# Kernel optimization log

Hardware: AMD Instinct MI355X
Metric: run time of the kernel (lower is better)

The kernel has to match this reference:

```python
import jax, jax.numpy as jnp
import numpy as np

DEC_HIDDEN = 512


def setup_inputs() -> dict:
    key = jax.random.key(0)
    k1, k2, k3, k4 = jax.random.split(key, 4)
    B, S, DEC, ENC2 = 32, 2048, 512, 1024
    s = jax.random.normal(k1, (1, B, DEC), dtype=jnp.float32)
    enc_output = jax.random.normal(k2, (B, S, ENC2), dtype=jnp.float32)
    # nn.Linear weights: attn [dec_hidden, enc_hidden*2 + dec_hidden], v [1, dec_hidden]
    W_attn = jax.random.normal(k3, (DEC, DEC + ENC2), dtype=jnp.float32) * (1.0 / np.sqrt(DEC + ENC2))
    W_v = jax.random.normal(k4, (1, DEC), dtype=jnp.float32) * (1.0 / np.sqrt(DEC))
    return {"s": s, "enc_output": enc_output, "W_attn": W_attn, "W_v": W_v}


def reference(s, enc_output, W_attn, W_v):
    # s: [1, B, D] -> [B, D]; enc_output: [B, S, 2E]
    s = jnp.squeeze(s, axis=0)
    dec = s.shape[-1]
    # torch.cat((s_repeated, enc_output), dim=2) @ W_attn.T, computed without
    # materializing the repeat/concat: split W_attn by column blocks.
    W_s = W_attn[:, :dec]       # [D, D]   (columns matching s)
    W_e = W_attn[:, dec:]       # [D, 2E]  (columns matching enc_output)
    # energy: [B, S, D]
    energy = jnp.tanh(
        jnp.einsum('bd,hd->bh', s, W_s)[:, None, :]
        + jnp.einsum('bse,he->bsh', enc_output, W_e)
    )
    # atten: [B, S]
    atten = jnp.einsum('bsh,h->bs', energy, W_v[0])
    soft_attn_weights = jax.nn.softmax(atten, axis=1)
    # context: [B, 2E]
    context = jnp.einsum('bs,bse->be', soft_attn_weights, enc_output)
    return (context, soft_attn_weights)
```

## Files before the change

### kernel.cpp

```cpp
#include <hip/hip_runtime.h>
#include <hip/hip_bf16.h>


typedef __attribute__((ext_vector_type(8))) short bf16x8;
typedef __attribute__((ext_vector_type(4))) float f32x4;

#define SB0() __builtin_amdgcn_sched_barrier(0)

static __device__ __forceinline__ unsigned short f2bf(float f) {
    union { float f; unsigned u; } v; v.f = f;
    unsigned r = (v.u + 0x7fffu + ((v.u >> 16) & 1u)) >> 16;
    return (unsigned short)r;
}

static __device__ __forceinline__ unsigned pk2(float x, float y) {
    union { __hip_bfloat162 h; unsigned u; } c;
    c.h = __float22bfloat162_rn(make_float2(x, y));
    return c.u;
}

static __device__ __forceinline__ float fast_tanh(float x) {
    return 1.0f - 2.0f / (__expf(2.0f * x) + 1.0f);
}

__global__ __launch_bounds__(256) void prep_sw(const float* __restrict__ s,
                                               const float* __restrict__ Wat,
                                               float* __restrict__ sW) {
    int id = blockIdx.x * 256 + threadIdx.x;
    int b = id >> 9, h = id & 511;
    const float4* wr = (const float4*)(Wat + (size_t)h * 1536);
    const float4* sr = (const float4*)(s + (size_t)b * 512);
    float acc = 0.f;
#pragma unroll 8
    for (int i = 0; i < 128; ++i) {
        float4 w = wr[i], sv = sr[i];
        acc += w.x * sv.x + w.y * sv.y + w.z * sv.z + w.w * sv.w;
    }
    sW[id] = acc;
}

__global__ __launch_bounds__(256) void prep_weB(const float* __restrict__ Wat,
                                                unsigned short* __restrict__ WebfB) {
    int tid = blockIdx.x * 256 + threadIdx.x;
    int lane = tid & 63;
    int g = tid >> 6;
    int nf = g & 3, wc = (g >> 2) & 3, kk = (g >> 4) & 1, step = (g >> 5) & 15, ct = (g >> 9) & 1;
    int col = ct * 256 + wc * 64 + nf * 16 + (lane & 15);
    int k0 = step * 64 + kk * 32 + (lane >> 4) * 8;
    const float* src = Wat + (size_t)col * 1536 + 512 + k0;
    float4 w0 = *(const float4*)src;
    float4 w1 = *(const float4*)(src + 4);
    union { unsigned short us[8]; int4 v; } p;
    p.us[0] = f2bf(w0.x); p.us[1] = f2bf(w0.y); p.us[2] = f2bf(w0.z); p.us[3] = f2bf(w0.w);
    p.us[4] = f2bf(w1.x); p.us[5] = f2bf(w1.y); p.us[6] = f2bf(w1.z); p.us[7] = f2bf(w1.w);
    *(int4*)(WebfB + (size_t)tid * 8) = p.v;
}

__global__ __launch_bounds__(256, 3) void energy_kernel(
    const float* __restrict__ enc, const unsigned short* __restrict__ WebfB,
    const float* __restrict__ sW, const float* __restrict__ Wv,
    float* __restrict__ attpart) {
    __shared__ __align__(16) unsigned short lT0[4096];
    __shared__ __align__(16) unsigned short lT1[4096];
    __shared__ float lred[4][64];

    const int t = threadIdx.x;
    const int lane = t & 63;
    const int wc = t >> 6;
    const int bid = blockIdx.x;
    const int ct = (bid >> 3) & 1;
    const int rt = (bid & 7) | ((bid >> 4) << 3);
    const int m0 = rt * 64;
    const int b = m0 >> 11;
    const int l15 = lane & 15;
    const int lkg = lane >> 4;

    const int arow = t >> 4;
    const int achk = t & 15;
    const float* aptr = enc + (size_t)(m0 + arow) * 1024 + achk * 4;
    const int wsw = (((achk >> 1) ^ (arow & 7)) << 4) | ((achk & 1) << 3);

    const int rrowbase = l15 * 128;
    const int rsw0 = (lkg ^ (l15 & 7)) << 4;
    const int rsw1 = ((4 + lkg) ^ (l15 & 7)) << 4;

    const unsigned short* wBbase = WebfB + (size_t)ct * 262144 + lane * 8;

    f32x4 acc[4][4];
#pragma unroll
    for (int mf = 0; mf < 4; ++mf)
#pragma unroll
        for (int nf = 0; nf < 4; ++nf) acc[mf][nf] = (f32x4){0.f, 0.f, 0.f, 0.f};

    float4 aregA[4], aregB[4];
    bf16x8 bfr[8];

#define LOADA(STEP, AR)                                                        \
    do {                                                                       \
        _Pragma("unroll")                                                      \
        for (int q = 0; q < 4; ++q)                                            \
            AR[q] = *(const float4*)(aptr + (size_t)q * 16384 + (STEP) * 64);  \
    } while (0)

#define LOADB(I)                                                               \
    do {                                                                       \
        _Pragma("unroll")                                                      \
        for (int kk = 0; kk < 2; ++kk)                                         \
            _Pragma("unroll")                                                  \
            for (int nf = 0; nf < 4; ++nf)                                     \
                bfr[kk * 4 + nf] = *(const bf16x8*)(                           \
                    wBbase + (size_t)((((I) * 2 + kk) * 4 + wc) * 4 + nf) * 512); \
    } while (0)

#define CVTW(AR, BUF)                                                          \
    do {                                                                       \
        _Pragma("unroll")                                                      \
        for (int q = 0; q < 4; ++q) {                                          \
            uint2 wv;                                                          \
            wv.x = pk2(AR[q].x, AR[q].y);                                      \
            wv.y = pk2(AR[q].z, AR[q].w);                                      \
            *(uint2*)((char*)(BUF) + (q * 16 + arow) * 128 + wsw) = wv;        \
        }                                                                      \
    } while (0)

#define COMP(BUF)                                                              \
    do {                                                                       \
        _Pragma("unroll")                                                      \
        for (int kk = 0; kk < 2; ++kk) {                                       \
            const int rs = kk ? rsw1 : rsw0;                                   \
            _Pragma("unroll")                                                  \
            for (int mf = 0; mf < 4; ++mf) {                                   \
                bf16x8 af = *(const bf16x8*)((const char*)(BUF) + rrowbase +   \
                                             mf * 2048 + rs);                  \
                _Pragma("unroll")                                              \
                for (int nf = 0; nf < 4; ++nf)                                 \
                    acc[mf][nf] = __builtin_amdgcn_mfma_f32_16x16x32_bf16(     \
                        af, bfr[kk * 4 + nf], acc[mf][nf], 0, 0, 0);           \
            }                                                                  \
        }                                                                      \
    } while (0)

#define BARRIER()                                              \
    do {                                                       \
        asm volatile("s_waitcnt lgkmcnt(0)" ::: "memory");     \
        __builtin_amdgcn_s_barrier();                          \
    } while (0)

#define STEP_FULL(I, CUR, NXT, AUSE, ALOAD)    \
    do {                                       \
        LOADB(I); SB0();                       \
        LOADA((I) + 2, ALOAD); SB0();          \
        CVTW(AUSE, NXT); SB0();                \
        __builtin_amdgcn_s_setprio(1);         \
        COMP(CUR);                             \
        __builtin_amdgcn_s_setprio(0);         \
        BARRIER();                             \
    } while (0)

    LOADA(0, aregA); SB0();
    LOADA(1, aregB); SB0();
    CVTW(aregA, lT0);
    BARRIER();

#pragma unroll 1
    for (int i = 0; i < 14; i += 2) {
        STEP_FULL(i, lT0, lT1, aregB, aregA);
        STEP_FULL(i + 1, lT1, lT0, aregA, aregB);
    }
    LOADB(14); SB0();
    CVTW(aregB, lT1); SB0();
    __builtin_amdgcn_s_setprio(1);
    COMP(lT0);
    __builtin_amdgcn_s_setprio(0);
    BARRIER();
    LOADB(15); SB0();
    __builtin_amdgcn_s_setprio(1);
    COMP(lT1);
    __builtin_amdgcn_s_setprio(0);

    float sWv[4], wvv[4];
#pragma unroll
    for (int nf = 0; nf < 4; ++nf) {
        int col = ct * 256 + wc * 64 + nf * 16 + l15;
        sWv[nf] = sW[(b << 9) + col];
        wvv[nf] = Wv[col];
    }
    float pa[4][4];
#pragma unroll
    for (int mf = 0; mf < 4; ++mf) {
#pragma unroll
        for (int r = 0; r < 4; ++r) pa[mf][r] = 0.f;
#pragma unroll
        for (int nf = 0; nf < 4; ++nf)
#pragma unroll
            for (int r = 0; r < 4; ++r)
                pa[mf][r] += fast_tanh(acc[mf][nf][r] + sWv[nf]) * wvv[nf];
    }
#pragma unroll
    for (int m = 1; m < 16; m <<= 1)
#pragma unroll
        for (int mf = 0; mf < 4; ++mf)
#pragma unroll
            for (int r = 0; r < 4; ++r)
                pa[mf][r] += __shfl_xor(pa[mf][r], m, 64);

    if (l15 == 0) {
#pragma unroll
        for (int mf = 0; mf < 4; ++mf)
#pragma unroll
            for (int r = 0; r < 4; ++r)
                lred[wc][mf * 16 + lkg * 4 + r] = pa[mf][r];
    }
    __syncthreads();
    if (t < 64) {
        attpart[(size_t)ct * 65536 + m0 + t] =
            (lred[0][t] + lred[1][t]) + (lred[2][t] + lred[3][t]);
    }
#undef LOADA
#undef LOADB
#undef CVTW
#undef COMP
#undef BARRIER
#undef STEP_FULL
}

__global__ __launch_bounds__(256) void softmax_kernel(const float* __restrict__ attpart,
                                                      float* __restrict__ out) {
    int b = blockIdx.x, t = threadIdx.x;
    float v[8];
#pragma unroll
    for (int i = 0; i < 8; ++i) {
        int idx = b * 2048 + t + 256 * i;
        v[i] = attpart[idx] + attpart[65536 + idx];
    }
    float mx = v[0];
#pragma unroll
    for (int i = 1; i < 8; ++i) mx = fmaxf(mx, v[i]);
#pragma unroll
    for (int m = 1; m < 64; m <<= 1) mx = fmaxf(mx, __shfl_xor(mx, m, 64));
    __shared__ float redm[4], reds[4];
    if ((t & 63) == 0) redm[t >> 6] = mx;
    __syncthreads();
    mx = fmaxf(fmaxf(redm[0], redm[1]), fmaxf(redm[2], redm[3]));
    float sum = 0.f;
#pragma unroll
    for (int i = 0; i < 8; ++i) { v[i] = __expf(v[i] - mx); sum += v[i]; }
#pragma unroll
    for (int m = 1; m < 64; m <<= 1) sum += __shfl_xor(sum, m, 64);
    if ((t & 63) == 0) reds[t >> 6] = sum;
    __syncthreads();
    sum = reds[0] + reds[1] + reds[2] + reds[3];
    float inv = 1.0f / sum;
    float* soft = out + 32768;
#pragma unroll
    for (int i = 0; i < 8; ++i) soft[b * 2048 + t + 256 * i] = v[i] * inv;
}

__global__ __launch_bounds__(256) void ctx_partial(const float* __restrict__ enc,
                                                   const float* __restrict__ soft,
                                                   float* __restrict__ part) {
    int blk = blockIdx.x;
    int b = blk >> 4, s0 = (blk & 15) * 128;
    int t = threadIdx.x;
    float4 a = {0.f, 0.f, 0.f, 0.f};
    const float* base = enc + ((size_t)(b * 2048 + s0)) * 1024 + t * 4;
    const float* sw = soft + b * 2048 + s0;
#pragma unroll 4
    for (int s = 0; s < 128; ++s) {
        float w = sw[s];
        float4 e = *(const float4*)(base + (size_t)s * 1024);
        a.x += w * e.x; a.y += w * e.y; a.z += w * e.z; a.w += w * e.w;
    }
    *(float4*)(part + (size_t)blk * 1024 + t * 4) = a;
}

__global__ __launch_bounds__(256) void ctx_reduce(const float* __restrict__ part,
                                                  float* __restrict__ ctx) {
    int id = blockIdx.x * 256 + threadIdx.x;
    int b = id >> 10, e = id & 1023;
    float s = 0.f;
#pragma unroll 8
    for (int c = 0; c < 16; ++c) s += part[((size_t)(b * 16 + c)) * 1024 + e];
    ctx[id] = s;
}

extern "C" void kernel_launch(void* const* d_in, const int* in_sizes, int n_in,
                              void* d_out, int out_size, void* d_ws, size_t ws_size,
                              hipStream_t stream) {
    const float* s   = (const float*)d_in[0];
    const float* enc = (const float*)d_in[1];
    const float* Wat = (const float*)d_in[2];
    const float* Wv  = (const float*)d_in[3];
    float* out = (float*)d_out;

    char* ws = (char*)d_ws;
    float* sW             = (float*)ws;
    unsigned short* WebfB = (unsigned short*)(ws + (64 << 10));
    float* attpart        = (float*)(ws + (64 << 10) + (1 << 20));
    float* part           = (float*)(ws + (64 << 10) + (1 << 20) + (512 << 10));

    prep_sw<<<64, 256, 0, stream>>>(s, Wat, sW);
    prep_weB<<<2048, 256, 0, stream>>>(Wat, WebfB);
    energy_kernel<<<2048, 256, 0, stream>>>(enc, WebfB, sW, Wv, attpart);
    softmax_kernel<<<32, 256, 0, stream>>>(attpart, out);
    ctx_partial<<<512, 256, 0, stream>>>(enc, out + 32768, part);
    ctx_reduce<<<128, 256, 0, stream>>>(part, out);
}
```

Before: 168.1 us.

## Stage energy-kernel weight tiles into LDS via async global_load_lds double buffering

```diff
diff --git a/kernel.cpp b/kernel.cpp
--- a/kernel.cpp
+++ b/kernel.cpp
@@ -4,8 +4,12 @@
 
 typedef __attribute__((ext_vector_type(8))) short bf16x8;
 typedef __attribute__((ext_vector_type(4))) float f32x4;
+typedef __attribute__((address_space(3))) unsigned lds_u32;
+typedef const __attribute__((address_space(1))) unsigned g_u32;
 
 #define SB0() __builtin_amdgcn_sched_barrier(0)
+#define PRIO1 __builtin_amdgcn_s_setprio(1)
+#define PRIO0 __builtin_amdgcn_s_setprio(0)
 
 static __device__ __forceinline__ unsigned short f2bf(float f) {
     union { float f; unsigned u; } v; v.f = f;
@@ -56,13 +60,16 @@
     *(int4*)(WebfB + (size_t)tid * 8) = p.v;
 }
 
-__global__ __launch_bounds__(256, 3) void energy_kernel(
+__global__ __launch_bounds__(256, 2) void energy_kernel(
     const float* __restrict__ enc, const unsigned short* __restrict__ WebfB,
     const float* __restrict__ sW, const float* __restrict__ Wv,
     float* __restrict__ attpart) {
-    __shared__ __align__(16) unsigned short lT0[4096];
-    __shared__ __align__(16) unsigned short lT1[4096];
-    __shared__ float lred[4][64];
+    __shared__ __align__(16) char smem[81920];
+    unsigned short* lT0 = (unsigned short*)smem;
+    unsigned short* lT1 = (unsigned short*)(smem + 8192);
+    char* Bb0 = smem + 16384;
+    char* Bb1 = smem + 49152;
+    float* lred = (float*)smem;
 
     const int t = threadIdx.x;
     const int lane = t & 63;
@@ -84,7 +91,7 @@
     const int rsw0 = (lkg ^ (l15 & 7)) << 4;
     const int rsw1 = ((4 + lkg) ^ (l15 & 7)) << 4;
 
-    const unsigned short* wBbase = WebfB + (size_t)ct * 262144 + lane * 8;
+    const char* gB = (const char*)WebfB + (size_t)ct * 524288;
 
     f32x4 acc[4][4];
 #pragma unroll
@@ -92,91 +99,88 @@
 #pragma unroll
         for (int nf = 0; nf < 4; ++nf) acc[mf][nf] = (f32x4){0.f, 0.f, 0.f, 0.f};
 
-    float4 aregA[4], aregB[4];
-    bf16x8 bfr[8];
-
-#define LOADA(STEP, AR)                                                        \
+    float4 azA[4], azB[4];
+
+#define BSTAGE(I, BB)                                                          \
+    do {                                                                       \
+        _Pragma("unroll")                                                      \
+        for (int q = 0; q < 8; ++q)                                            \
+            __builtin_amdgcn_global_load_lds(                                  \
+                (g_u32*)(gB + (size_t)(I) * 32768 + q * 4096 + wc * 1024 +     \
+                         lane * 16),                                           \
+                (lds_u32*)((BB) + q * 4096 + wc * 1024), 16, 0, 0);            \
+    } while (0)
+
+#define LOADA(S, AR)                                                           \
     do {                                                                       \
         _Pragma("unroll")                                                      \
         for (int q = 0; q < 4; ++q)                                            \
-            AR[q] = *(const float4*)(aptr + (size_t)q * 16384 + (STEP) * 64);  \
-    } while (0)
-
-#define LOADB(I)                                                               \
-    do {                                                                       \
-        _Pragma("unroll")                                                      \
-        for (int kk = 0; kk < 2; ++kk)                                         \
-            _Pragma("unroll")                                                  \
-            for (int nf = 0; nf < 4; ++nf)                                     \
-                bfr[kk * 4 + nf] = *(const bf16x8*)(                           \
-                    wBbase + (size_t)((((I) * 2 + kk) * 4 + wc) * 4 + nf) * 512); \
-    } while (0)
-
-#define CVTW(AR, BUF)                                                          \
+            AR[q] = *(const float4*)(aptr + (size_t)q * 16384 + (S) * 64);     \
+    } while (0)
+
+#define CVTW(AR, LT)                                                           \
     do {                                                                       \
         _Pragma("unroll")                                                      \
         for (int q = 0; q < 4; ++q) {                                          \
             uint2 wv;                                                          \
             wv.x = pk2(AR[q].x, AR[q].y);                                      \
             wv.y = pk2(AR[q].z, AR[q].w);                                      \
-            *(uint2*)((char*)(BUF) + (q * 16 + arow) * 128 + wsw) = wv;        \
+            *(uint2*)((char*)(LT) + (q * 16 + arow) * 128 + wsw) = wv;         \
         }                                                                      \
     } while (0)
 
-#define COMP(BUF)                                                              \
+#define COMP(LT, BB)                                                           \
     do {                                                                       \
         _Pragma("unroll")                                                      \
         for (int kk = 0; kk < 2; ++kk) {                                       \
             const int rs = kk ? rsw1 : rsw0;                                   \
             _Pragma("unroll")                                                  \
             for (int mf = 0; mf < 4; ++mf) {                                   \
-                bf16x8 af = *(const bf16x8*)((const char*)(BUF) + rrowbase +   \
+                bf16x8 af = *(const bf16x8*)((const char*)(LT) + rrowbase +    \
                                              mf * 2048 + rs);                  \
                 _Pragma("unroll")                                              \
-                for (int nf = 0; nf < 4; ++nf)                                 \
+                for (int nf = 0; nf < 4; ++nf) {                               \
+                    bf16x8 bf = *(const bf16x8*)(                              \
+                        (BB) + (kk * 16 + wc * 4 + nf) * 1024 + lane * 16);    \
                     acc[mf][nf] = __builtin_amdgcn_mfma_f32_16x16x32_bf16(     \
-                        af, bfr[kk * 4 + nf], acc[mf][nf], 0, 0, 0);           \
+                        af, bf, acc[mf][nf], 0, 0, 0);                         \
+                }                                                              \
             }                                                                  \
         }                                                                      \
     } while (0)
 
-#define BARRIER()                                              \
-    do {                                                       \
-        asm volatile("s_waitcnt lgkmcnt(0)" ::: "memory");     \
-        __builtin_amdgcn_s_barrier();                          \
-    } while (0)
-
-#define STEP_FULL(I, CUR, NXT, AUSE, ALOAD)    \
-    do {                                       \
-        LOADB(I); SB0();                       \
-        LOADA((I) + 2, ALOAD); SB0();          \
-        CVTW(AUSE, NXT); SB0();                \
-        __builtin_amdgcn_s_setprio(1);         \
-        COMP(CUR);                             \
-        __builtin_amdgcn_s_setprio(0);         \
-        BARRIER();                             \
-    } while (0)
-
-    LOADA(0, aregA); SB0();
-    LOADA(1, aregB); SB0();
-    CVTW(aregA, lT0);
-    BARRIER();
+#define ENDSTEP(N)                                                             \
+    do {                                                                       \
+        asm volatile("s_waitcnt vmcnt(" #N ") lgkmcnt(0)" ::: "memory");       \
+        SB0();                                                                 \
+        __builtin_amdgcn_s_barrier();                                          \
+    } while (0)
+
+    BSTAGE(0, Bb0); SB0();
+    LOADA(0, azA); SB0();
+    LOADA(1, azB); SB0();
+    CVTW(azA, lT0);
+    ENDSTEP(4);
 
 #pragma unroll 1
-    for (int i = 0; i < 14; i += 2) {
-        STEP_FULL(i, lT0, lT1, aregB, aregA);
-        STEP_FULL(i + 1, lT1, lT0, aregA, aregB);
-    }
-    LOADB(14); SB0();
-    CVTW(aregB, lT1); SB0();
-    __builtin_amdgcn_s_setprio(1);
-    COMP(lT0);
-    __builtin_amdgcn_s_setprio(0);
-    BARRIER();
-    LOADB(15); SB0();
-    __builtin_amdgcn_s_setprio(1);
-    COMP(lT1);
-    __builtin_amdgcn_s_setprio(0);
+    for (int k = 0; k < 7; ++k) {
+        const int i = 2 * k;
+        BSTAGE(i + 1, Bb1); SB0();
+        LOADA(i + 2, azA); SB0();
+        CVTW(azB, lT1); SB0();
+        PRIO1; COMP(lT0, Bb0); PRIO0;
+        ENDSTEP(4);
+        BSTAGE(i + 2, Bb0); SB0();
+        LOADA(i + 3, azB); SB0();
+        CVTW(azA, lT0); SB0();
+        PRIO1; COMP(lT1, Bb1); PRIO0;
+        ENDSTEP(4);
+    }
+    BSTAGE(15, Bb1); SB0();
+    CVTW(azB, lT1); SB0();
+    PRIO1; COMP(lT0, Bb0); PRIO0;
+    ENDSTEP(0);
+    PRIO1; COMP(lT1, Bb1); PRIO0;
 
     float sWv[4], wvv[4];
 #pragma unroll
@@ -204,24 +208,25 @@
             for (int r = 0; r < 4; ++r)
                 pa[mf][r] += __shfl_xor(pa[mf][r], m, 64);
 
+    __syncthreads();
     if (l15 == 0) {
 #pragma unroll
         for (int mf = 0; mf < 4; ++mf)
 #pragma unroll
             for (int r = 0; r < 4; ++r)
-                lred[wc][mf * 16 + lkg * 4 + r] = pa[mf][r];
+                lred[wc * 64 + mf * 16 + lkg * 4 + r] = pa[mf][r];
     }
     __syncthreads();
     if (t < 64) {
         attpart[(size_t)ct * 65536 + m0 + t] =
-            (lred[0][t] + lred[1][t]) + (lred[2][t] + lred[3][t]);
-    }
+            (lred[0 * 64 + t] + lred[1 * 64 + t]) +
+            (lred[2 * 64 + t] + lred[3 * 64 + t]);
+    }
+#undef BSTAGE
 #undef LOADA
-#undef LOADB
 #undef CVTW
 #undef COMP
-#undef BARRIER
-#undef STEP_FULL
+#undef ENDSTEP
 }
 
 __global__ __launch_bounds__(256) void softmax_kernel(const float* __restrict__ attpart,
@@ -300,7 +305,7 @@
     float* part           = (float*)(ws + (64 << 10) + (1 << 20) + (512 << 10));
 
     prep_sw<<<64, 256, 0, stream>>>(s, Wat, sW);
-    prep_weB<<<2048, 256, 0, stream>>>(Wat, WebfB);
+    prep_weB<<<256, 256, 0, stream>>>(Wat, WebfB);
     energy_kernel<<<2048, 256, 0, stream>>>(enc, WebfB, sW, Wv, attpart);
     softmax_kernel<<<32, 256, 0, stream>>>(attpart, out);
     ctx_partial<<<512, 256, 0, stream>>>(enc, out + 32768, part);
```

Result: slower. 190.5 us (+13.3%).

## Shrink energy tile to 64x128 with two-wave blocks and trim prep_weB grid

Applied to the files above, without the earlier changes.

```diff
diff --git a/kernel.cpp b/kernel.cpp
--- a/kernel.cpp
+++ b/kernel.cpp
@@ -6,6 +6,8 @@
 typedef __attribute__((ext_vector_type(4))) float f32x4;
 
 #define SB0() __builtin_amdgcn_sched_barrier(0)
+#define PRIO1 __builtin_amdgcn_s_setprio(1)
+#define PRIO0 __builtin_amdgcn_s_setprio(0)
 
 static __device__ __forceinline__ unsigned short f2bf(float f) {
     union { float f; unsigned u; } v; v.f = f;
@@ -56,35 +58,37 @@
     *(int4*)(WebfB + (size_t)tid * 8) = p.v;
 }
 
-__global__ __launch_bounds__(256, 3) void energy_kernel(
+__global__ __launch_bounds__(128, 4) void energy_kernel(
     const float* __restrict__ enc, const unsigned short* __restrict__ WebfB,
     const float* __restrict__ sW, const float* __restrict__ Wv,
     float* __restrict__ attpart) {
     __shared__ __align__(16) unsigned short lT0[4096];
     __shared__ __align__(16) unsigned short lT1[4096];
-    __shared__ float lred[4][64];
+    __shared__ float lred[2][64];
 
     const int t = threadIdx.x;
     const int lane = t & 63;
     const int wc = t >> 6;
     const int bid = blockIdx.x;
-    const int ct = (bid >> 3) & 1;
-    const int rt = (bid & 7) | ((bid >> 4) << 3);
+    const int ct = (bid >> 3) & 3;
+    const int rt = (bid & 7) | ((bid >> 5) << 3);
     const int m0 = rt * 64;
     const int b = m0 >> 11;
     const int l15 = lane & 15;
     const int lkg = lane >> 4;
+    const int ct2 = ct >> 1;
+    const int wc4 = (ct & 1) * 2 + wc;
 
     const int arow = t >> 4;
     const int achk = t & 15;
     const float* aptr = enc + (size_t)(m0 + arow) * 1024 + achk * 4;
-    const int wsw = (((achk >> 1) ^ (arow & 7)) << 4) | ((achk & 1) << 3);
+    const int wsw = (((achk >> 1) ^ arow) << 4) | ((achk & 1) << 3);
 
     const int rrowbase = l15 * 128;
     const int rsw0 = (lkg ^ (l15 & 7)) << 4;
     const int rsw1 = ((4 + lkg) ^ (l15 & 7)) << 4;
 
-    const unsigned short* wBbase = WebfB + (size_t)ct * 262144 + lane * 8;
+    const unsigned short* wB = WebfB + (size_t)ct2 * 262144 + lane * 8;
 
     f32x4 acc[4][4];
 #pragma unroll
@@ -92,14 +96,14 @@
 #pragma unroll
         for (int nf = 0; nf < 4; ++nf) acc[mf][nf] = (f32x4){0.f, 0.f, 0.f, 0.f};
 
-    float4 aregA[4], aregB[4];
+    float4 areg[8];
     bf16x8 bfr[8];
 
-#define LOADA(STEP, AR)                                                        \
-    do {                                                                       \
-        _Pragma("unroll")                                                      \
-        for (int q = 0; q < 4; ++q)                                            \
-            AR[q] = *(const float4*)(aptr + (size_t)q * 16384 + (STEP) * 64);  \
+#define LOADA(S)                                                               \
+    do {                                                                       \
+        _Pragma("unroll")                                                      \
+        for (int q = 0; q < 8; ++q)                                            \
+            areg[q] = *(const float4*)(aptr + (size_t)q * 8192 + (S) * 64);    \
     } while (0)
 
 #define LOADB(I)                                                               \
@@ -109,28 +113,28 @@
             _Pragma("unroll")                                                  \
             for (int nf = 0; nf < 4; ++nf)                                     \
                 bfr[kk * 4 + nf] = *(const bf16x8*)(                           \
-                    wBbase + (size_t)((((I) * 2 + kk) * 4 + wc) * 4 + nf) * 512); \
-    } while (0)
-
-#define CVTW(AR, BUF)                                                          \
-    do {                                                                       \
-        _Pragma("unroll")                                                      \
-        for (int q = 0; q < 4; ++q) {                                          \
+                    wB + (size_t)((((I) * 2 + kk) * 4 + wc4) * 4 + nf) * 512); \
+    } while (0)
+
+#define CVTW(LT)                                                               \
+    do {                                                                       \
+        _Pragma("unroll")                                                      \
+        for (int q = 0; q < 8; ++q) {                                          \
             uint2 wv;                                                          \
-            wv.x = pk2(AR[q].x, AR[q].y);                                      \
-            wv.y = pk2(AR[q].z, AR[q].w);                                      \
-            *(uint2*)((char*)(BUF) + (q * 16 + arow) * 128 + wsw) = wv;        \
+            wv.x = pk2(areg[q].x, areg[q].y);                                  \
+            wv.y = pk2(areg[q].z, areg[q].w);                                  \
+            *(uint2*)((char*)(LT) + (q * 8 + arow) * 128 + wsw) = wv;          \
         }                                                                      \
     } while (0)
 
-#define COMP(BUF)                                                              \
+#define COMP(LT)                                                               \
     do {                                                                       \
         _Pragma("unroll")                                                      \
         for (int kk = 0; kk < 2; ++kk) {                                       \
             const int rs = kk ? rsw1 : rsw0;                                   \
             _Pragma("unroll")                                                  \
             for (int mf = 0; mf < 4; ++mf) {                                   \
-                bf16x8 af = *(const bf16x8*)((const char*)(BUF) + rrowbase +   \
+                bf16x8 af = *(const bf16x8*)((const char*)(LT) + rrowbase +    \
                                              mf * 2048 + rs);                  \
                 _Pragma("unroll")                                              \
                 for (int nf = 0; nf < 4; ++nf)                                 \
@@ -146,42 +150,29 @@
         __builtin_amdgcn_s_barrier();                          \
     } while (0)
 
-#define STEP_FULL(I, CUR, NXT, AUSE, ALOAD)    \
-    do {                                       \
-        LOADB(I); SB0();                       \
-        LOADA((I) + 2, ALOAD); SB0();          \
-        CVTW(AUSE, NXT); SB0();                \
-        __builtin_amdgcn_s_setprio(1);         \
-        COMP(CUR);                             \
-        __builtin_amdgcn_s_setprio(0);         \
-        BARRIER();                             \
-    } while (0)
-
-    LOADA(0, aregA); SB0();
-    LOADA(1, aregB); SB0();
-    CVTW(aregA, lT0);
+    LOADA(0); SB0();
+    CVTW(lT0);
+    LOADA(1); SB0();
     BARRIER();
 
+    unsigned short* cur = lT0;
+    unsigned short* nxt = lT1;
 #pragma unroll 1
-    for (int i = 0; i < 14; i += 2) {
-        STEP_FULL(i, lT0, lT1, aregB, aregA);
-        STEP_FULL(i + 1, lT1, lT0, aregA, aregB);
-    }
-    LOADB(14); SB0();
-    CVTW(aregB, lT1); SB0();
-    __builtin_amdgcn_s_setprio(1);
-    COMP(lT0);
-    __builtin_amdgcn_s_setprio(0);
-    BARRIER();
+    for (int i = 0; i < 15; ++i) {
+        LOADB(i); SB0();
+        CVTW(nxt); SB0();
+        if (i < 14) { LOADA(i + 2); SB0(); }
+        PRIO1; COMP(cur); PRIO0;
+        BARRIER();
+        { unsigned short* tp = cur; cur = nxt; nxt = tp; }
+    }
     LOADB(15); SB0();
-    __builtin_amdgcn_s_setprio(1);
-    COMP(lT1);
-    __builtin_amdgcn_s_setprio(0);
+    PRIO1; COMP(cur); PRIO0;
 
     float sWv[4], wvv[4];
 #pragma unroll
     for (int nf = 0; nf < 4; ++nf) {
-        int col = ct * 256 + wc * 64 + nf * 16 + l15;
+        int col = ct * 128 + wc * 64 + nf * 16 + l15;
         sWv[nf] = sW[(b << 9) + col];
         wvv[nf] = Wv[col];
     }
@@ -213,15 +204,13 @@
     }
     __syncthreads();
     if (t < 64) {
-        attpart[(size_t)ct * 65536 + m0 + t] =
-            (lred[0][t] + lred[1][t]) + (lred[2][t] + lred[3][t]);
+        attpart[(size_t)ct * 65536 + m0 + t] = lred[0][t] + lred[1][t];
     }
 #undef LOADA
 #undef LOADB
 #undef CVTW
 #undef COMP
 #undef BARRIER
-#undef STEP_FULL
 }
 
 __global__ __launch_bounds__(256) void softmax_kernel(const float* __restrict__ attpart,
@@ -231,7 +220,8 @@
 #pragma unroll
     for (int i = 0; i < 8; ++i) {
         int idx = b * 2048 + t + 256 * i;
-        v[i] = attpart[idx] + attpart[65536 + idx];
+        v[i] = (attpart[idx] + attpart[65536 + idx]) +
+               (attpart[131072 + idx] + attpart[196608 + idx]);
     }
     float mx = v[0];
 #pragma unroll
@@ -297,11 +287,11 @@
     float* sW             = (float*)ws;
     unsigned short* WebfB = (unsigned short*)(ws + (64 << 10));
     float* attpart        = (float*)(ws + (64 << 10) + (1 << 20));
-    float* part           = (float*)(ws + (64 << 10) + (1 << 20) + (512 << 10));
+    float* part           = (float*)(ws + (64 << 10) + (2 << 20));
 
     prep_sw<<<64, 256, 0, stream>>>(s, Wat, sW);
-    prep_weB<<<2048, 256, 0, stream>>>(Wat, WebfB);
-    energy_kernel<<<2048, 256, 0, stream>>>(enc, WebfB, sW, Wv, attpart);
+    prep_weB<<<256, 256, 0, stream>>>(Wat, WebfB);
+    energy_kernel<<<4096, 128, 0, stream>>>(enc, WebfB, sW, Wv, attpart);
     softmax_kernel<<<32, 256, 0, stream>>>(attpart, out);
     ctx_partial<<<512, 256, 0, stream>>>(enc, out + 32768, part);
     ctx_reduce<<<128, 256, 0, stream>>>(part, out);
```

Result: slower. 520.6 us (+209.7%).
